# Kernel tuning notes

Measured on AMD Instinct MI355X. Metric: run time of the kernel, lower is better.

The kernel has to match this reference:

```python
import jax, jax.numpy as jnp
import numpy as np

B, N, D, E, ET, L = 2, 50000, 64, 400000, 200000, 6
R_STRUCT = 4
EPS = 1e-5


def _ln(x, g, b):
    m = jnp.mean(x, axis=-1, keepdims=True)
    v = jnp.mean((x - m) ** 2, axis=-1, keepdims=True)
    return (x - m) * jax.lax.rsqrt(v + EPS) * g + b


def _nbf(boundary, src, dst, rel_e_fn, W, b, g, beta):
    # One RelNBFNet / TextRelNBFNet stack of GeneralizedRelationalConv layers:
    #   distmult message, sum aggregation with boundary self-loop message,
    #   linear([x, agg]) -> layernorm -> relu, short_cut residual.
    # boundary: [B, N, D]
    x = boundary
    for i in range(W.shape[0]):
        msg = x[:, src, :] * rel_e_fn(i)                    # [B, E, D]
        agg = jnp.zeros_like(x).at[:, dst, :].add(msg) + boundary
        h = jnp.concatenate([x, agg], axis=-1) @ W[i] + b[i]
        h = jax.nn.relu(_ln(h, g[i], beta[i]))
        x = h + x                                           # short_cut
    return x


def setup_inputs() -> dict:
    key = jax.random.key(0)
    ks = jax.random.split(key, 16)
    s = 0.05
    return {
        "rel_text_init": jax.random.normal(ks[0], (N, D), jnp.float32),
        "struct_rel": jax.random.normal(ks[1], (L, R_STRUCT, D), jnp.float32) * s,
        "struct_W": jax.random.normal(ks[2], (L, 2 * D, D), jnp.float32) * s,
        "struct_b": jnp.zeros((L, D), jnp.float32),
        "struct_g": jnp.ones((L, D), jnp.float32),
        "struct_beta": jnp.zeros((L, D), jnp.float32),
        "text_rel": jax.random.normal(ks[3], (L, 1, D), jnp.float32) * s,
        "text_W": jax.random.normal(ks[4], (L, 2 * D, D), jnp.float32) * s,
        "text_b": jnp.zeros((L, D), jnp.float32),
        "text_g": jnp.ones((L, D), jnp.float32),
        "text_beta": jnp.zeros((L, D), jnp.float32),
        "fuse_W1": jax.random.normal(ks[5], (2 * D, D), jnp.float32) * s,
        "fuse_b1": jnp.zeros((D,), jnp.float32),
        "fuse_W2": jax.random.normal(ks[6], (D, D), jnp.float32) * s,
        "fuse_b2": jnp.zeros((D,), jnp.float32),
        "h_index": jax.random.randint(ks[7], (B,), 0, N),
        "edge_index": jax.random.randint(ks[8], (2, E), 0, N),
        "edge_type": jax.random.randint(ks[9], (E,), 0, R_STRUCT),
        "text_edge_index": jax.random.randint(ks[10], (2, ET), 0, N),
    }


def reference(rel_text_init, struct_rel, struct_W, struct_b, struct_g, struct_beta,
              text_rel, text_W, text_b, text_g, text_beta,
              fuse_W1, fuse_b1, fuse_W2, fuse_b2,
              h_index, edge_index, edge_type, text_edge_index):
    # struct branch: boundary = indicator at query relation node
    boundary_s = jnp.zeros((B, N, D), rel_text_init.dtype).at[jnp.arange(B), h_index].add(1.0)
    h = _nbf(boundary_s, edge_index[0], edge_index[1],
             lambda i: struct_rel[i][edge_type],
             struct_W, struct_b, struct_g, struct_beta)
    # text branch: boundary = text-derived init features, single relation type
    boundary_t = jnp.broadcast_to(rel_text_init[None], (B, N, D))
    z = _nbf(boundary_t, text_edge_index[0], text_edge_index[1],
             lambda i: text_rel[i, 0][None, None, :],
             text_W, text_b, text_g, text_beta)
    # mlp fusion (alpha = 1.0)
    f = jax.nn.relu(jnp.concatenate([h, z], axis=-1) @ fuse_W1 + fuse_b1)
    return f @ fuse_W2 + fuse_b2
```

## Files before the change

kernel.cpp:

```cpp
#include <hip/hip_runtime.h>


#define FMA4R(v, wbase, R0, R1, R2, R3) do {                                  \
    const float4* _w = (const float4*)(wbase); float4 _t;                     \
    _t=_w[0]; R0.x=fmaf(v,_t.x,R0.x); R0.y=fmaf(v,_t.y,R0.y); R0.z=fmaf(v,_t.z,R0.z); R0.w=fmaf(v,_t.w,R0.w); \
    _t=_w[1]; R1.x=fmaf(v,_t.x,R1.x); R1.y=fmaf(v,_t.y,R1.y); R1.z=fmaf(v,_t.z,R1.z); R1.w=fmaf(v,_t.w,R1.w); \
    _t=_w[2]; R2.x=fmaf(v,_t.x,R2.x); R2.y=fmaf(v,_t.y,R2.y); R2.z=fmaf(v,_t.z,R2.z); R2.w=fmaf(v,_t.w,R2.w); \
    _t=_w[3]; R3.x=fmaf(v,_t.x,R3.x); R3.y=fmaf(v,_t.y,R3.y); R3.z=fmaf(v,_t.z,R3.z); R3.w=fmaf(v,_t.w,R3.w); \
} while (0)

#define SUM4(Ai) ((Ai.x + Ai.y) + (Ai.z + Ai.w))
#define VAR4(Ai) do { float _c;                                               \
    _c = Ai.x - m; vs = fmaf(_c, _c, vs); _c = Ai.y - m; vs = fmaf(_c, _c, vs); \
    _c = Ai.z - m; vs = fmaf(_c, _c, vs); _c = Ai.w - m; vs = fmaf(_c, _c, vs); \
} while (0)

#define RSEL(ty) (((ty) < 2) ? ((ty) == 0 ? r0 : r1) : ((ty) == 2 ? r2 : r3))

__global__ __launch_bounds__(256) void k_init_onehot(
    float* __restrict__ x, const int* __restrict__ h_index, int N, int total)
{
    int idx = blockIdx.x * 256 + threadIdx.x;
    if (idx >= total) return;
    int row = idx >> 6;
    int b = row / N;
    int n = row - b * N;
    x[idx] = (n == h_index[b]) ? 1.0f : 0.0f;
}

__global__ __launch_bounds__(256) void k_hist(
    const int* __restrict__ dst, int* __restrict__ cnt, int E)
{
    int e = blockIdx.x * 256 + threadIdx.x;
    if (e < E) atomicAdd(&cnt[dst[e]], 1);
}

__global__ __launch_bounds__(1024) void k_scan_blk(
    const int* __restrict__ cnt, int* __restrict__ off,
    int* __restrict__ bsum, int n)
{
    __shared__ int wsum[16], wpre[16], tot;
    int tid = threadIdx.x, lane = tid & 63, w = tid >> 6;
    int i = blockIdx.x * 1024 + tid;
    int v = (i < n) ? cnt[i] : 0;
    int s = v;
    #pragma unroll
    for (int d = 1; d < 64; d <<= 1) {
        int t = __shfl_up(s, d);
        if (lane >= d) s += t;
    }
    if (lane == 63) wsum[w] = s;
    __syncthreads();
    if (w == 0 && lane < 16) {
        int ws = wsum[lane];
        int p = ws;
        #pragma unroll
        for (int d = 1; d < 16; d <<= 1) {
            int t = __shfl_up(p, d);
            if (lane >= d) p += t;
        }
        wpre[lane] = p - ws;
        if (lane == 15) tot = p;
    }
    __syncthreads();
    if (i < n) off[i + 1] = wpre[w] + s;
    if (tid == 0) {
        bsum[blockIdx.x] = tot;
        if (blockIdx.x == 0) off[0] = 0;
    }
}

__global__ __launch_bounds__(1024) void k_scan_top(int* __restrict__ bsum, int nb)
{
    __shared__ int wsum[16], wpre[16];
    int tid = threadIdx.x, lane = tid & 63, w = tid >> 6;
    int v = (tid < nb) ? bsum[tid] : 0;
    int s = v;
    #pragma unroll
    for (int d = 1; d < 64; d <<= 1) {
        int t = __shfl_up(s, d);
        if (lane >= d) s += t;
    }
    if (lane == 63) wsum[w] = s;
    __syncthreads();
    if (w == 0 && lane < 16) {
        int ws = wsum[lane];
        int p = ws;
        #pragma unroll
        for (int d = 1; d < 16; d <<= 1) {
            int t = __shfl_up(p, d);
            if (lane >= d) p += t;
        }
        wpre[lane] = p - ws;
    }
    __syncthreads();
    if (tid < nb) bsum[tid] = wpre[w] + s - v;
}

__global__ __launch_bounds__(1024) void k_scan_add(
    const int* __restrict__ bsum, int* __restrict__ off, int n)
{
    int i = blockIdx.x * 1024 + threadIdx.x;
    if (i < n) off[i + 1] += bsum[blockIdx.x];
}

__global__ __launch_bounds__(256) void k_fill(
    const int* __restrict__ src, const int* __restrict__ dst,
    const int* __restrict__ etype,
    const int* __restrict__ off, int* __restrict__ cnt,
    int* __restrict__ packed, int E)
{
    int e = blockIdx.x * 256 + threadIdx.x;
    if (e >= E) return;
    int d = dst[e];
    int pos = off[d] + atomicSub(&cnt[d], 1) - 1;
    int ty = etype ? etype[e] : 0;
    packed[pos] = src[e] | (ty << 27);
}

__global__ __launch_bounds__(256) void k_gather_struct2(
    const float* __restrict__ x, float* __restrict__ agg,
    const int* __restrict__ off, const int* __restrict__ packed,
    const float* __restrict__ rel,
    const int* __restrict__ h_index,
    int N)
{
    int n = (blockIdx.x * 256 + threadIdx.x) >> 6;
    int lane = threadIdx.x & 63;
    if (n >= N) return;
    float r0 = rel[lane], r1 = rel[64 + lane];
    float r2 = rel[128 + lane], r3 = rel[192 + lane];
    const float* x0 = x;
    const float* x1 = x + (size_t)N * 64;
    float acc0 = (n == h_index[0]) ? 1.0f : 0.0f;
    float acc1 = (n == h_index[1]) ? 1.0f : 0.0f;
    int p0 = __builtin_amdgcn_readfirstlane(off[n]);
    int p1 = __builtin_amdgcn_readfirstlane(off[n + 1]);
    for (int p = p0; p < p1; p += 64) {
        int myPk = (p + lane < p1) ? packed[p + lane] : 0;
        int cnt = min(p1 - p, 64);
        int i = 0;
        for (; i + 4 <= cnt; i += 4) {
            int pka = __shfl(myPk, i + 0), pkb = __shfl(myPk, i + 1);
            int pkc = __shfl(myPk, i + 2), pkd = __shfl(myPk, i + 3);
            int sa = pka & 0x03FFFFFF, ta = pka >> 27;
            int sb = pkb & 0x03FFFFFF, tb = pkb >> 27;
            int sc = pkc & 0x03FFFFFF, tc = pkc >> 27;
            int sd = pkd & 0x03FFFFFF, td = pkd >> 27;
            float ra = RSEL(ta), rb = RSEL(tb), rc = RSEL(tc), rd = RSEL(td);
            float a0 = x0[(size_t)sa * 64 + lane], a1 = x1[(size_t)sa * 64 + lane];
            float b0 = x0[(size_t)sb * 64 + lane], b1 = x1[(size_t)sb * 64 + lane];
            float c0 = x0[(size_t)sc * 64 + lane], c1 = x1[(size_t)sc * 64 + lane];
            float d0 = x0[(size_t)sd * 64 + lane], d1 = x1[(size_t)sd * 64 + lane];
            acc0 = fmaf(a0, ra, acc0); acc1 = fmaf(a1, ra, acc1);
            acc0 = fmaf(b0, rb, acc0); acc1 = fmaf(b1, rb, acc1);
            acc0 = fmaf(c0, rc, acc0); acc1 = fmaf(c1, rc, acc1);
            acc0 = fmaf(d0, rd, acc0); acc1 = fmaf(d1, rd, acc1);
        }
        for (; i < cnt; ++i) {
            int pk = __shfl(myPk, i);
            int s = pk & 0x03FFFFFF, ty = pk >> 27;
            float r = RSEL(ty);
            acc0 = fmaf(x0[(size_t)s * 64 + lane], r, acc0);
            acc1 = fmaf(x1[(size_t)s * 64 + lane], r, acc1);
        }
    }
    agg[(size_t)n * 64 + lane] = acc0;
    agg[(size_t)(N + n) * 64 + lane] = acc1;
}

__global__ __launch_bounds__(256) void k_gather_struct_gen(
    const float* __restrict__ x, float* __restrict__ agg,
    const int* __restrict__ off, const int* __restrict__ packed,
    const float* __restrict__ rel, const int* __restrict__ h_index,
    int N, int BN)
{
    int wid = (blockIdx.x * 256 + threadIdx.x) >> 6;
    int lane = threadIdx.x & 63;
    if (wid >= BN) return;
    int b = wid / N;
    int n = wid - b * N;
    float r0 = rel[lane], r1 = rel[64 + lane];
    float r2 = rel[128 + lane], r3 = rel[192 + lane];
    const float* xb = x + (size_t)b * N * 64;
    float acc = (n == h_index[b]) ? 1.0f : 0.0f;
    int p0 = off[n], p1 = off[n + 1];
    for (int p = p0; p < p1; ++p) {
        int pk = packed[p];
        int s = pk & 0x03FFFFFF, ty = pk >> 27;
        acc = fmaf(xb[(size_t)s * 64 + lane], RSEL(ty), acc);
    }
    agg[(size_t)wid * 64 + lane] = acc;
}

__global__ __launch_bounds__(256) void k_gather_text(
    const float* __restrict__ x, float* __restrict__ agg,
    const int* __restrict__ off, const int* __restrict__ packed,
    const float* __restrict__ rel,
    const float* __restrict__ init,
    int N)
{
    int n = (blockIdx.x * 256 + threadIdx.x) >> 6;
    int lane = threadIdx.x & 63;
    if (n >= N) return;
    float r = rel[lane];
    float acc = init[(size_t)n * 64 + lane];
    float acc2 = 0.f;
    int p0 = __builtin_amdgcn_readfirstlane(off[n]);
    int p1 = __builtin_amdgcn_readfirstlane(off[n + 1]);
    for (int p = p0; p < p1; p += 64) {
        int myPk = (p + lane < p1) ? packed[p + lane] : 0;
        int cnt = min(p1 - p, 64);
        int i = 0;
        for (; i + 4 <= cnt; i += 4) {
            int sa = __shfl(myPk, i + 0), sb = __shfl(myPk, i + 1);
            int sc = __shfl(myPk, i + 2), sd = __shfl(myPk, i + 3);
            float a = x[(size_t)sa * 64 + lane];
            float b = x[(size_t)sb * 64 + lane];
            float c = x[(size_t)sc * 64 + lane];
            float d = x[(size_t)sd * 64 + lane];
            acc = fmaf(a, r, acc);  acc2 = fmaf(b, r, acc2);
            acc = fmaf(c, r, acc);  acc2 = fmaf(d, r, acc2);
        }
        for (; i < cnt; ++i) {
            int s = __shfl(myPk, i);
            acc = fmaf(x[(size_t)s * 64 + lane], r, acc);
        }
    }
    agg[(size_t)n * 64 + lane] = acc + acc2;
}

__global__ __launch_bounds__(256) void k_update(
    const float* __restrict__ W,
    const float* __restrict__ bias, const float* __restrict__ g,
    const float* __restrict__ beta,
    float* __restrict__ x, const float* __restrict__ agg, int rows)
{
    __shared__ float Wl[128 * 64];
    __shared__ float bl[64], gl[64], bel[64];
    int tid = threadIdx.x;
    {
        const float4* W4 = (const float4*)W;
        float4* Wl4 = (float4*)Wl;
        #pragma unroll
        for (int i = 0; i < 8; ++i) Wl4[tid + i * 256] = W4[tid + i * 256];
        if (tid < 64) { bl[tid] = bias[tid]; gl[tid] = g[tid]; bel[tid] = beta[tid]; }
    }
    __syncthreads();

    int gt = blockIdx.x * 256 + tid;
    int row = gt >> 2;
    int jc = (gt & 3) * 16;
    if (row >= rows) return;
    const float* xr = x + (size_t)row * 64;
    const float* ar = agg + (size_t)row * 64;

    const float4* bj = (const float4*)(bl + jc);
    float4 A0 = bj[0], A1 = bj[1], A2 = bj[2], A3 = bj[3];

    #pragma unroll
    for (int kb = 0; kb < 64; kb += 4) {
        float4 iv = *(const float4*)(xr + kb);
        FMA4R(iv.x, Wl + (kb + 0) * 64 + jc, A0, A1, A2, A3);
        FMA4R(iv.y, Wl + (kb + 1) * 64 + jc, A0, A1, A2, A3);
        FMA4R(iv.z, Wl + (kb + 2) * 64 + jc, A0, A1, A2, A3);
        FMA4R(iv.w, Wl + (kb + 3) * 64 + jc, A0, A1, A2, A3);
    }
    #pragma unroll
    for (int kb = 0; kb < 64; kb += 4) {
        float4 iv = *(const float4*)(ar + kb);
        FMA4R(iv.x, Wl + (64 + kb + 0) * 64 + jc, A0, A1, A2, A3);
        FMA4R(iv.y, Wl + (64 + kb + 1) * 64 + jc, A0, A1, A2, A3);
        FMA4R(iv.z, Wl + (64 + kb + 2) * 64 + jc, A0, A1, A2, A3);
        FMA4R(iv.w, Wl + (64 + kb + 3) * 64 + jc, A0, A1, A2, A3);
    }

    float ls = SUM4(A0) + SUM4(A1) + SUM4(A2) + SUM4(A3);
    ls += __shfl_xor(ls, 1);
    ls += __shfl_xor(ls, 2);
    float m = ls * (1.0f / 64.0f);
    float vs = 0.f;
    VAR4(A0); VAR4(A1); VAR4(A2); VAR4(A3);
    vs += __shfl_xor(vs, 1);
    vs += __shfl_xor(vs, 2);
    float inv = rsqrtf(vs * (1.0f / 64.0f) + 1e-5f);

    float* xw = x + (size_t)row * 64 + jc;
    const float4* gg4 = (const float4*)(gl + jc);
    const float4* bb4 = (const float4*)(bel + jc);
    const float4* xv4 = (const float4*)(xr + jc);
    #define OUTC(Aj, c) do {                                                  \
        float4 xv = xv4[c]; float4 gg = gg4[c]; float4 bb = bb4[c];           \
        float4 y;                                                             \
        y.x = fmaxf((Aj.x - m) * inv * gg.x + bb.x, 0.f) + xv.x;              \
        y.y = fmaxf((Aj.y - m) * inv * gg.y + bb.y, 0.f) + xv.y;              \
        y.z = fmaxf((Aj.z - m) * inv * gg.z + bb.z, 0.f) + xv.z;              \
        y.w = fmaxf((Aj.w - m) * inv * gg.w + bb.w, 0.f) + xv.w;              \
        ((float4*)xw)[c] = y; } while (0)
    OUTC(A0, 0); OUTC(A1, 1); OUTC(A2, 2); OUTC(A3, 3);
    #undef OUTC
}

__global__ __launch_bounds__(256) void k_fuse(
    const float* __restrict__ W1, const float* __restrict__ b1,
    const float* __restrict__ W2, const float* __restrict__ b2,
    float* __restrict__ out, const float* __restrict__ z, int N, int rows)
{
    __shared__ float W1l[128 * 64];
    __shared__ float W2l[64 * 64];
    __shared__ float b1l[64], b2l[64];
    int tid = threadIdx.x;
    {
        const float4* Wa = (const float4*)W1;
        float4* Wla = (float4*)W1l;
        #pragma unroll
        for (int i = 0; i < 8; ++i) Wla[tid + i * 256] = Wa[tid + i * 256];
        const float4* Wb = (const float4*)W2;
        float4* Wlb = (float4*)W2l;
        #pragma unroll
        for (int i = 0; i < 4; ++i) Wlb[tid + i * 256] = Wb[tid + i * 256];
        if (tid < 64) { b1l[tid] = b1[tid]; b2l[tid] = b2[tid]; }
    }
    __syncthreads();

    int gt = blockIdx.x * 256 + tid;
    int row = gt >> 2;
    int q = gt & 3;
    int jc = q * 16;
    if (row >= rows) return;
    int n = row % N;
    const float* hr = out + (size_t)row * 64;
    const float* zr = z + (size_t)n * 64;
    int lane = tid & 63;

    const float4* bj = (const float4*)(b1l + jc);
    float4 F0 = bj[0], F1 = bj[1], F2 = bj[2], F3 = bj[3];
    #pragma unroll
    for (int kb = 0; kb < 64; kb += 4) {
        float4 iv = *(const float4*)(hr + kb);
        FMA4R(iv.x, W1l + (kb + 0) * 64 + jc, F0, F1, F2, F3);
        FMA4R(iv.y, W1l + (kb + 1) * 64 + jc, F0, F1, F2, F3);
        FMA4R(iv.z, W1l + (kb + 2) * 64 + jc, F0, F1, F2, F3);
        FMA4R(iv.w, W1l + (kb + 3) * 64 + jc, F0, F1, F2, F3);
    }
    #pragma unroll
    for (int kb = 0; kb < 64; kb += 4) {
        float4 iv = *(const float4*)(zr + kb);
        FMA4R(iv.x, W1l + (64 + kb + 0) * 64 + jc, F0, F1, F2, F3);
        FMA4R(iv.y, W1l + (64 + kb + 1) * 64 + jc, F0, F1, F2, F3);
        FMA4R(iv.z, W1l + (64 + kb + 2) * 64 + jc, F0, F1, F2, F3);
        FMA4R(iv.w, W1l + (64 + kb + 3) * 64 + jc, F0, F1, F2, F3);
    }
    F0.x = fmaxf(F0.x, 0.f); F0.y = fmaxf(F0.y, 0.f); F0.z = fmaxf(F0.z, 0.f); F0.w = fmaxf(F0.w, 0.f);
    F1.x = fmaxf(F1.x, 0.f); F1.y = fmaxf(F1.y, 0.f); F1.z = fmaxf(F1.z, 0.f); F1.w = fmaxf(F1.w, 0.f);
    F2.x = fmaxf(F2.x, 0.f); F2.y = fmaxf(F2.y, 0.f); F2.z = fmaxf(F2.z, 0.f); F2.w = fmaxf(F2.w, 0.f);
    F3.x = fmaxf(F3.x, 0.f); F3.y = fmaxf(F3.y, 0.f); F3.z = fmaxf(F3.z, 0.f); F3.w = fmaxf(F3.w, 0.f);

    const float4* bj2 = (const float4*)(b2l + jc);
    float4 O0 = bj2[0], O1 = bj2[1], O2 = bj2[2], O3 = bj2[3];
    int srcLane = (lane & ~3) | ((q + 1) & 3);
    #pragma unroll
    for (int s = 0; s < 4; ++s) {
        int c = (q + s) & 3;
        const float* w2 = W2l + (c * 16) * 64 + jc;
        FMA4R(F0.x, w2 + 0 * 64,  O0, O1, O2, O3);
        FMA4R(F0.y, w2 + 1 * 64,  O0, O1, O2, O3);
        FMA4R(F0.z, w2 + 2 * 64,  O0, O1, O2, O3);
        FMA4R(F0.w, w2 + 3 * 64,  O0, O1, O2, O3);
        FMA4R(F1.x, w2 + 4 * 64,  O0, O1, O2, O3);
        FMA4R(F1.y, w2 + 5 * 64,  O0, O1, O2, O3);
        FMA4R(F1.z, w2 + 6 * 64,  O0, O1, O2, O3);
        FMA4R(F1.w, w2 + 7 * 64,  O0, O1, O2, O3);
        FMA4R(F2.x, w2 + 8 * 64,  O0, O1, O2, O3);
        FMA4R(F2.y, w2 + 9 * 64,  O0, O1, O2, O3);
        FMA4R(F2.z, w2 + 10 * 64, O0, O1, O2, O3);
        FMA4R(F2.w, w2 + 11 * 64, O0, O1, O2, O3);
        FMA4R(F3.x, w2 + 12 * 64, O0, O1, O2, O3);
        FMA4R(F3.y, w2 + 13 * 64, O0, O1, O2, O3);
        FMA4R(F3.z, w2 + 14 * 64, O0, O1, O2, O3);
        FMA4R(F3.w, w2 + 15 * 64, O0, O1, O2, O3);
        if (s < 3) {
            F0.x = __shfl(F0.x, srcLane); F0.y = __shfl(F0.y, srcLane);
            F0.z = __shfl(F0.z, srcLane); F0.w = __shfl(F0.w, srcLane);
            F1.x = __shfl(F1.x, srcLane); F1.y = __shfl(F1.y, srcLane);
            F1.z = __shfl(F1.z, srcLane); F1.w = __shfl(F1.w, srcLane);
            F2.x = __shfl(F2.x, srcLane); F2.y = __shfl(F2.y, srcLane);
            F2.z = __shfl(F2.z, srcLane); F2.w = __shfl(F2.w, srcLane);
            F3.x = __shfl(F3.x, srcLane); F3.y = __shfl(F3.y, srcLane);
            F3.z = __shfl(F3.z, srcLane); F3.w = __shfl(F3.w, srcLane);
        }
    }
    float4* ow4 = (float4*)(out + (size_t)row * 64 + jc);
    ow4[0] = O0; ow4[1] = O1; ow4[2] = O2; ow4[3] = O3;
}

extern "C" void kernel_launch(void* const* d_in, const int* in_sizes, int n_in,
                              void* d_out, int out_size, void* d_ws, size_t ws_size,
                              hipStream_t stream)
{
    const float* rel_text_init = (const float*)d_in[0];
    const float* struct_rel    = (const float*)d_in[1];
    const float* struct_W      = (const float*)d_in[2];
    const float* struct_b      = (const float*)d_in[3];
    const float* struct_g      = (const float*)d_in[4];
    const float* struct_beta   = (const float*)d_in[5];
    const float* text_rel      = (const float*)d_in[6];
    const float* text_W        = (const float*)d_in[7];
    const float* text_b        = (const float*)d_in[8];
    const float* text_g        = (const float*)d_in[9];
    const float* text_beta     = (const float*)d_in[10];
    const float* fuse_W1       = (const float*)d_in[11];
    const float* fuse_b1       = (const float*)d_in[12];
    const float* fuse_W2       = (const float*)d_in[13];
    const float* fuse_b2       = (const float*)d_in[14];
    const int*   h_index       = (const int*)d_in[15];
    const int*   edge_index    = (const int*)d_in[16];
    const int*   edge_type     = (const int*)d_in[17];
    const int*   text_edge_idx = (const int*)d_in[18];

    const int B  = in_sizes[15];
    const int N  = in_sizes[0] / 64;
    const int E  = in_sizes[17];
    const int ET = in_sizes[18] / 2;
    const int L  = in_sizes[3] / 64;
    const int R  = in_sizes[1] / (L * 64);

    const int* src  = edge_index;
    const int* dst  = edge_index + E;
    const int* tsrc = text_edge_idx;
    const int* tdst = text_edge_idx + ET;

    float* x_t   = (float*)d_ws;
    float* agg_t = x_t + (size_t)N * 64;
    float* agg_s = agg_t + (size_t)N * 64;
    int*   cnt_s = (int*)(agg_s + (size_t)B * N * 64);
    int*   off_s = cnt_s + N;
    int*   pk_s  = off_s + N + 1;
    int*   cnt_t = pk_s + E;
    int*   off_t = cnt_t + N;
    int*   pk_t  = off_t + N + 1;
    int*   bsum_s = pk_t + ET;
    int*   bsum_t = bsum_s + 1024;

    float* x_s = (float*)d_out;

    const size_t nd  = (size_t)N * 64;
    const int rows_s = B * N;
    const int tot_s  = rows_s * 64;
    const int nb     = (N + 1023) / 1024;

    const int gb_init   = (tot_s + 255) / 256;
    const int gb_e      = (E + 255) / 256;
    const int gb_et     = (ET + 255) / 256;
    const int gb_wave_n = (N * 64 + 255) / 256;
    const int gb_upd_s  = (rows_s * 4 + 255) / 256;
    const int gb_upd_t  = (N * 4 + 255) / 256;
    const int gb_fuse   = (rows_s * 4 + 255) / 256;

    hipMemsetAsync(cnt_s, 0, (size_t)N * 4, stream);
    hipMemsetAsync(cnt_t, 0, (size_t)N * 4, stream);
    k_hist<<<gb_e, 256, 0, stream>>>(dst, cnt_s, E);
    k_hist<<<gb_et, 256, 0, stream>>>(tdst, cnt_t, ET);
    k_scan_blk<<<nb, 1024, 0, stream>>>(cnt_s, off_s, bsum_s, N);
    k_scan_blk<<<nb, 1024, 0, stream>>>(cnt_t, off_t, bsum_t, N);
    k_scan_top<<<1, 1024, 0, stream>>>(bsum_s, nb);
    k_scan_top<<<1, 1024, 0, stream>>>(bsum_t, nb);
    k_scan_add<<<nb, 1024, 0, stream>>>(bsum_s, off_s, N);
    k_scan_add<<<nb, 1024, 0, stream>>>(bsum_t, off_t, N);
    k_fill<<<gb_e, 256, 0, stream>>>(src, dst, edge_type, off_s, cnt_s, pk_s, E);
    k_fill<<<gb_et, 256, 0, stream>>>(tsrc, tdst, nullptr, off_t, cnt_t, pk_t, ET);

    k_init_onehot<<<gb_init, 256, 0, stream>>>(x_s, h_index, N, tot_s);
    for (int i = 0; i < L; ++i) {
        if (B == 2) {
            k_gather_struct2<<<gb_wave_n, 256, 0, stream>>>(
                x_s, agg_s, off_s, pk_s,
                struct_rel + (size_t)i * R * 64, h_index, N);
        } else {
            k_gather_struct_gen<<<(rows_s * 64 + 255) / 256, 256, 0, stream>>>(
                x_s, agg_s, off_s, pk_s,
                struct_rel + (size_t)i * R * 64, h_index, N, rows_s);
        }
        k_update<<<gb_upd_s, 256, 0, stream>>>(
            struct_W + (size_t)i * 128 * 64, struct_b + i * 64,
            struct_g + i * 64, struct_beta + i * 64, x_s, agg_s, rows_s);
    }

    hipMemcpyAsync(x_t, rel_text_init, nd * sizeof(float),
                   hipMemcpyDeviceToDevice, stream);
    for (int i = 0; i < L; ++i) {
        k_gather_text<<<gb_wave_n, 256, 0, stream>>>(
            x_t, agg_t, off_t, pk_t,
            text_rel + (size_t)i * 64, rel_text_init, N);
        k_update<<<gb_upd_t, 256, 0, stream>>>(
            text_W + (size_t)i * 128 * 64, text_b + i * 64,
            text_g + i * 64, text_beta + i * 64, x_t, agg_t, N);
    }

    k_fuse<<<gb_fuse, 256, 0, stream>>>(
        fuse_W1, fuse_b1, fuse_W2, fuse_b2, x_s, x_t, N, rows_s);
}
```

Before: 800.2 us.

## Co-launch struct and text branches per layer and process two rows per thread

Measured after the change: 956.8 us. +19.6%, slower.

```diff
diff --git a/kernel.cpp b/kernel.cpp
--- a/kernel.cpp
+++ b/kernel.cpp
@@ -9,10 +9,26 @@
     _t=_w[3]; R3.x=fmaf(v,_t.x,R3.x); R3.y=fmaf(v,_t.y,R3.y); R3.z=fmaf(v,_t.z,R3.z); R3.w=fmaf(v,_t.w,R3.w); \
 } while (0)
 
+#define FMA4R2(v0, v1, wbase, P0,P1,P2,P3, Q0,Q1,Q2,Q3) do {                  \
+    const float4* _w = (const float4*)(wbase); float4 _t;                     \
+    _t=_w[0];                                                                 \
+    P0.x=fmaf(v0,_t.x,P0.x); P0.y=fmaf(v0,_t.y,P0.y); P0.z=fmaf(v0,_t.z,P0.z); P0.w=fmaf(v0,_t.w,P0.w); \
+    Q0.x=fmaf(v1,_t.x,Q0.x); Q0.y=fmaf(v1,_t.y,Q0.y); Q0.z=fmaf(v1,_t.z,Q0.z); Q0.w=fmaf(v1,_t.w,Q0.w); \
+    _t=_w[1];                                                                 \
+    P1.x=fmaf(v0,_t.x,P1.x); P1.y=fmaf(v0,_t.y,P1.y); P1.z=fmaf(v0,_t.z,P1.z); P1.w=fmaf(v0,_t.w,P1.w); \
+    Q1.x=fmaf(v1,_t.x,Q1.x); Q1.y=fmaf(v1,_t.y,Q1.y); Q1.z=fmaf(v1,_t.z,Q1.z); Q1.w=fmaf(v1,_t.w,Q1.w); \
+    _t=_w[2];                                                                 \
+    P2.x=fmaf(v0,_t.x,P2.x); P2.y=fmaf(v0,_t.y,P2.y); P2.z=fmaf(v0,_t.z,P2.z); P2.w=fmaf(v0,_t.w,P2.w); \
+    Q2.x=fmaf(v1,_t.x,Q2.x); Q2.y=fmaf(v1,_t.y,Q2.y); Q2.z=fmaf(v1,_t.z,Q2.z); Q2.w=fmaf(v1,_t.w,Q2.w); \
+    _t=_w[3];                                                                 \
+    P3.x=fmaf(v0,_t.x,P3.x); P3.y=fmaf(v0,_t.y,P3.y); P3.z=fmaf(v0,_t.z,P3.z); P3.w=fmaf(v0,_t.w,P3.w); \
+    Q3.x=fmaf(v1,_t.x,Q3.x); Q3.y=fmaf(v1,_t.y,Q3.y); Q3.z=fmaf(v1,_t.z,Q3.z); Q3.w=fmaf(v1,_t.w,Q3.w); \
+} while (0)
+
 #define SUM4(Ai) ((Ai.x + Ai.y) + (Ai.z + Ai.w))
-#define VAR4(Ai) do { float _c;                                               \
-    _c = Ai.x - m; vs = fmaf(_c, _c, vs); _c = Ai.y - m; vs = fmaf(_c, _c, vs); \
-    _c = Ai.z - m; vs = fmaf(_c, _c, vs); _c = Ai.w - m; vs = fmaf(_c, _c, vs); \
+#define VAR4M(Ai, mm, vv) do { float _c;                                      \
+    _c = Ai.x - mm; vv = fmaf(_c, _c, vv); _c = Ai.y - mm; vv = fmaf(_c, _c, vv); \
+    _c = Ai.z - mm; vv = fmaf(_c, _c, vv); _c = Ai.w - mm; vv = fmaf(_c, _c, vv); \
 } while (0)
 
 #define RSEL(ty) (((ty) < 2) ? ((ty) == 0 ? r0 : r1) : ((ty) == 2 ? r2 : r3))
@@ -28,20 +44,29 @@
     x[idx] = (n == h_index[b]) ? 1.0f : 0.0f;
 }
 
-__global__ __launch_bounds__(256) void k_hist(
-    const int* __restrict__ dst, int* __restrict__ cnt, int E)
-{
-    int e = blockIdx.x * 256 + threadIdx.x;
-    if (e < E) atomicAdd(&cnt[dst[e]], 1);
-}
-
-__global__ __launch_bounds__(1024) void k_scan_blk(
-    const int* __restrict__ cnt, int* __restrict__ off,
-    int* __restrict__ bsum, int n)
-{
+__global__ __launch_bounds__(256) void k_hist_all(
+    const int* __restrict__ dst_s, const int* __restrict__ dst_t,
+    int* __restrict__ cnt_s, int* __restrict__ cnt_t, int E, int ET)
+{
+    int i = blockIdx.x * 256 + threadIdx.x;
+    if (i < E) atomicAdd(&cnt_s[dst_s[i]], 1);
+    else if (i < E + ET) atomicAdd(&cnt_t[dst_t[i - E]], 1);
+}
+
+__global__ __launch_bounds__(1024) void k_scan_blk2(
+    const int* __restrict__ cnt_s, int* __restrict__ off_s, int* __restrict__ bsum_s,
+    const int* __restrict__ cnt_t, int* __restrict__ off_t, int* __restrict__ bsum_t,
+    int n, int nb)
+{
+    bool tpath = blockIdx.x >= nb;
+    int lb = tpath ? blockIdx.x - nb : blockIdx.x;
+    const int* cnt = tpath ? cnt_t : cnt_s;
+    int* off = tpath ? off_t : off_s;
+    int* bsum = tpath ? bsum_t : bsum_s;
+
     __shared__ int wsum[16], wpre[16], tot;
     int tid = threadIdx.x, lane = tid & 63, w = tid >> 6;
-    int i = blockIdx.x * 1024 + tid;
+    int i = lb * 1024 + tid;
     int v = (i < n) ? cnt[i] : 0;
     int s = v;
     #pragma unroll
@@ -65,13 +90,15 @@
     __syncthreads();
     if (i < n) off[i + 1] = wpre[w] + s;
     if (tid == 0) {
-        bsum[blockIdx.x] = tot;
-        if (blockIdx.x == 0) off[0] = 0;
-    }
-}
-
-__global__ __launch_bounds__(1024) void k_scan_top(int* __restrict__ bsum, int nb)
-{
+        bsum[lb] = tot;
+        if (lb == 0) off[0] = 0;
+    }
+}
+
+__global__ __launch_bounds__(1024) void k_scan_top2(
+    int* __restrict__ bsum_s, int* __restrict__ bsum_t, int nb)
+{
+    int* bsum = (blockIdx.x == 0) ? bsum_s : bsum_t;
     __shared__ int wsum[16], wpre[16];
     int tid = threadIdx.x, lane = tid & 63, w = tid >> 6;
     int v = (tid < nb) ? bsum[tid] : 0;
@@ -97,76 +124,128 @@
     if (tid < nb) bsum[tid] = wpre[w] + s - v;
 }
 
-__global__ __launch_bounds__(1024) void k_scan_add(
-    const int* __restrict__ bsum, int* __restrict__ off, int n)
-{
-    int i = blockIdx.x * 1024 + threadIdx.x;
-    if (i < n) off[i + 1] += bsum[blockIdx.x];
-}
-
-__global__ __launch_bounds__(256) void k_fill(
-    const int* __restrict__ src, const int* __restrict__ dst,
+__global__ __launch_bounds__(1024) void k_scan_add2(
+    const int* __restrict__ bsum_s, int* __restrict__ off_s,
+    const int* __restrict__ bsum_t, int* __restrict__ off_t, int n, int nb)
+{
+    bool tpath = blockIdx.x >= nb;
+    int lb = tpath ? blockIdx.x - nb : blockIdx.x;
+    int i = lb * 1024 + threadIdx.x;
+    if (i < n) (tpath ? off_t : off_s)[i + 1] += (tpath ? bsum_t : bsum_s)[lb];
+}
+
+__global__ __launch_bounds__(256) void k_fill_all(
+    const int* __restrict__ src_s, const int* __restrict__ dst_s,
     const int* __restrict__ etype,
-    const int* __restrict__ off, int* __restrict__ cnt,
-    int* __restrict__ packed, int E)
-{
-    int e = blockIdx.x * 256 + threadIdx.x;
-    if (e >= E) return;
-    int d = dst[e];
-    int pos = off[d] + atomicSub(&cnt[d], 1) - 1;
-    int ty = etype ? etype[e] : 0;
-    packed[pos] = src[e] | (ty << 27);
-}
-
-__global__ __launch_bounds__(256) void k_gather_struct2(
-    const float* __restrict__ x, float* __restrict__ agg,
-    const int* __restrict__ off, const int* __restrict__ packed,
-    const float* __restrict__ rel,
-    const int* __restrict__ h_index,
-    int N)
-{
-    int n = (blockIdx.x * 256 + threadIdx.x) >> 6;
-    int lane = threadIdx.x & 63;
+    const int* __restrict__ off_s, int* __restrict__ cnt_s, int* __restrict__ pk_s,
+    const int* __restrict__ src_t, const int* __restrict__ dst_t,
+    const int* __restrict__ off_t, int* __restrict__ cnt_t, int* __restrict__ pk_t,
+    int E, int ET)
+{
+    int i = blockIdx.x * 256 + threadIdx.x;
+    if (i < E) {
+        int d = dst_s[i];
+        int pos = off_s[d] + atomicSub(&cnt_s[d], 1) - 1;
+        pk_s[pos] = src_s[i] | (etype[i] << 27);
+    } else if (i < E + ET) {
+        int e = i - E;
+        int d = dst_t[e];
+        int pos = off_t[d] + atomicSub(&cnt_t[d], 1) - 1;
+        pk_t[pos] = src_t[e];
+    }
+}
+
+__global__ __launch_bounds__(256) void k_gather_all(
+    const float* __restrict__ xs, float* __restrict__ aggs,
+    const int* __restrict__ offs, const int* __restrict__ pks,
+    const float* __restrict__ rels,
+    const int* __restrict__ hidx,
+    const float* __restrict__ xt, float* __restrict__ aggt,
+    const int* __restrict__ offt, const int* __restrict__ pkt,
+    const float* __restrict__ relt,
+    const float* __restrict__ init,
+    int N, int sblocks, int tblocks)
+{
+    int tid = threadIdx.x;
+    int lane = tid & 63;
+    bool isStruct; int lb;
+    if (sblocks == tblocks) { isStruct = !(blockIdx.x & 1); lb = blockIdx.x >> 1; }
+    else if ((int)blockIdx.x < sblocks) { isStruct = true; lb = blockIdx.x; }
+    else { isStruct = false; lb = blockIdx.x - sblocks; }
+    int n = (lb * 256 + tid) >> 6;
     if (n >= N) return;
-    float r0 = rel[lane], r1 = rel[64 + lane];
-    float r2 = rel[128 + lane], r3 = rel[192 + lane];
-    const float* x0 = x;
-    const float* x1 = x + (size_t)N * 64;
-    float acc0 = (n == h_index[0]) ? 1.0f : 0.0f;
-    float acc1 = (n == h_index[1]) ? 1.0f : 0.0f;
-    int p0 = __builtin_amdgcn_readfirstlane(off[n]);
-    int p1 = __builtin_amdgcn_readfirstlane(off[n + 1]);
-    for (int p = p0; p < p1; p += 64) {
-        int myPk = (p + lane < p1) ? packed[p + lane] : 0;
-        int cnt = min(p1 - p, 64);
-        int i = 0;
-        for (; i + 4 <= cnt; i += 4) {
-            int pka = __shfl(myPk, i + 0), pkb = __shfl(myPk, i + 1);
-            int pkc = __shfl(myPk, i + 2), pkd = __shfl(myPk, i + 3);
-            int sa = pka & 0x03FFFFFF, ta = pka >> 27;
-            int sb = pkb & 0x03FFFFFF, tb = pkb >> 27;
-            int sc = pkc & 0x03FFFFFF, tc = pkc >> 27;
-            int sd = pkd & 0x03FFFFFF, td = pkd >> 27;
-            float ra = RSEL(ta), rb = RSEL(tb), rc = RSEL(tc), rd = RSEL(td);
-            float a0 = x0[(size_t)sa * 64 + lane], a1 = x1[(size_t)sa * 64 + lane];
-            float b0 = x0[(size_t)sb * 64 + lane], b1 = x1[(size_t)sb * 64 + lane];
-            float c0 = x0[(size_t)sc * 64 + lane], c1 = x1[(size_t)sc * 64 + lane];
-            float d0 = x0[(size_t)sd * 64 + lane], d1 = x1[(size_t)sd * 64 + lane];
-            acc0 = fmaf(a0, ra, acc0); acc1 = fmaf(a1, ra, acc1);
-            acc0 = fmaf(b0, rb, acc0); acc1 = fmaf(b1, rb, acc1);
-            acc0 = fmaf(c0, rc, acc0); acc1 = fmaf(c1, rc, acc1);
-            acc0 = fmaf(d0, rd, acc0); acc1 = fmaf(d1, rd, acc1);
+
+    if (isStruct) {
+        float r0 = rels[lane], r1 = rels[64 + lane];
+        float r2 = rels[128 + lane], r3 = rels[192 + lane];
+        const float* x0 = xs;
+        const float* x1 = xs + (size_t)N * 64;
+        float acc0 = (n == hidx[0]) ? 1.0f : 0.0f;
+        float acc1 = (n == hidx[1]) ? 1.0f : 0.0f;
+        int p0 = __builtin_amdgcn_readfirstlane(offs[n]);
+        int p1 = __builtin_amdgcn_readfirstlane(offs[n + 1]);
+        for (int p = p0; p < p1; p += 64) {
+            int myPk = (p + lane < p1) ? pks[p + lane] : 0;
+            int cnt = min(p1 - p, 64);
+            int i = 0;
+            for (; i + 4 <= cnt; i += 4) {
+                int pka = __shfl(myPk, i + 0), pkb = __shfl(myPk, i + 1);
+                int pkc = __shfl(myPk, i + 2), pkd = __shfl(myPk, i + 3);
+                int sa = pka & 0x03FFFFFF, ta = pka >> 27;
+                int sb = pkb & 0x03FFFFFF, tb = pkb >> 27;
+                int sc = pkc & 0x03FFFFFF, tc = pkc >> 27;
+                int sd = pkd & 0x03FFFFFF, td = pkd >> 27;
+                float ra = RSEL(ta), rb = RSEL(tb), rc = RSEL(tc), rd = RSEL(td);
+                float a0 = x0[(size_t)sa * 64 + lane], a1 = x1[(size_t)sa * 64 + lane];
+                float b0 = x0[(size_t)sb * 64 + lane], b1 = x1[(size_t)sb * 64 + lane];
+                float c0 = x0[(size_t)sc * 64 + lane], c1 = x1[(size_t)sc * 64 + lane];
+                float d0 = x0[(size_t)sd * 64 + lane], d1 = x1[(size_t)sd * 64 + lane];
+                acc0 = fmaf(a0, ra, acc0); acc1 = fmaf(a1, ra, acc1);
+                acc0 = fmaf(b0, rb, acc0); acc1 = fmaf(b1, rb, acc1);
+                acc0 = fmaf(c0, rc, acc0); acc1 = fmaf(c1, rc, acc1);
+                acc0 = fmaf(d0, rd, acc0); acc1 = fmaf(d1, rd, acc1);
+            }
+            for (; i < cnt; ++i) {
+                int pk = __shfl(myPk, i);
+                int s = pk & 0x03FFFFFF, ty = pk >> 27;
+                float r = RSEL(ty);
+                acc0 = fmaf(x0[(size_t)s * 64 + lane], r, acc0);
+                acc1 = fmaf(x1[(size_t)s * 64 + lane], r, acc1);
+            }
         }
-        for (; i < cnt; ++i) {
-            int pk = __shfl(myPk, i);
-            int s = pk & 0x03FFFFFF, ty = pk >> 27;
-            float r = RSEL(ty);
-            acc0 = fmaf(x0[(size_t)s * 64 + lane], r, acc0);
-            acc1 = fmaf(x1[(size_t)s * 64 + lane], r, acc1);
+        aggs[(size_t)n * 64 + lane] = acc0;
+        aggs[(size_t)(N + n) * 64 + lane] = acc1;
+    } else {
+        float r = relt[lane];
+        float acc = init[(size_t)n * 64 + lane];
+        float acc2 = 0.f;
+        int p0 = __builtin_amdgcn_readfirstlane(offt[n]);
+        int p1 = __builtin_amdgcn_readfirstlane(offt[n + 1]);
+        for (int p = p0; p < p1; p += 64) {
+            int myPk = (p + lane < p1) ? pkt[p + lane] : 0;
+            int cnt = min(p1 - p, 64);
+            int i = 0;
+            for (; i + 8 <= cnt; i += 8) {
+                int s0 = __shfl(myPk, i + 0), s1 = __shfl(myPk, i + 1);
+                int s2 = __shfl(myPk, i + 2), s3 = __shfl(myPk, i + 3);
+                int s4 = __shfl(myPk, i + 4), s5 = __shfl(myPk, i + 5);
+                int s6 = __shfl(myPk, i + 6), s7 = __shfl(myPk, i + 7);
+                float a = xt[(size_t)s0 * 64 + lane], b = xt[(size_t)s1 * 64 + lane];
+                float c = xt[(size_t)s2 * 64 + lane], d = xt[(size_t)s3 * 64 + lane];
+                float e = xt[(size_t)s4 * 64 + lane], f = xt[(size_t)s5 * 64 + lane];
+                float g = xt[(size_t)s6 * 64 + lane], h = xt[(size_t)s7 * 64 + lane];
+                acc = fmaf(a, r, acc);  acc2 = fmaf(b, r, acc2);
+                acc = fmaf(c, r, acc);  acc2 = fmaf(d, r, acc2);
+                acc = fmaf(e, r, acc);  acc2 = fmaf(f, r, acc2);
+                acc = fmaf(g, r, acc);  acc2 = fmaf(h, r, acc2);
+            }
+            for (; i < cnt; ++i) {
+                int s = __shfl(myPk, i);
+                acc = fmaf(xt[(size_t)s * 64 + lane], r, acc);
+            }
         }
-    }
-    agg[(size_t)n * 64 + lane] = acc0;
-    agg[(size_t)(N + n) * 64 + lane] = acc1;
+        aggt[(size_t)n * 64 + lane] = acc + acc2;
+    }
 }
 
 __global__ __launch_bounds__(256) void k_gather_struct_gen(
@@ -193,49 +272,31 @@
     agg[(size_t)wid * 64 + lane] = acc;
 }
 
-__global__ __launch_bounds__(256) void k_gather_text(
-    const float* __restrict__ x, float* __restrict__ agg,
-    const int* __restrict__ off, const int* __restrict__ packed,
-    const float* __restrict__ rel,
-    const float* __restrict__ init,
-    int N)
-{
-    int n = (blockIdx.x * 256 + threadIdx.x) >> 6;
-    int lane = threadIdx.x & 63;
-    if (n >= N) return;
-    float r = rel[lane];
-    float acc = init[(size_t)n * 64 + lane];
-    float acc2 = 0.f;
-    int p0 = __builtin_amdgcn_readfirstlane(off[n]);
-    int p1 = __builtin_amdgcn_readfirstlane(off[n + 1]);
-    for (int p = p0; p < p1; p += 64) {
-        int myPk = (p + lane < p1) ? packed[p + lane] : 0;
-        int cnt = min(p1 - p, 64);
-        int i = 0;
-        for (; i + 4 <= cnt; i += 4) {
-            int sa = __shfl(myPk, i + 0), sb = __shfl(myPk, i + 1);
-            int sc = __shfl(myPk, i + 2), sd = __shfl(myPk, i + 3);
-            float a = x[(size_t)sa * 64 + lane];
-            float b = x[(size_t)sb * 64 + lane];
-            float c = x[(size_t)sc * 64 + lane];
-            float d = x[(size_t)sd * 64 + lane];
-            acc = fmaf(a, r, acc);  acc2 = fmaf(b, r, acc2);
-            acc = fmaf(c, r, acc);  acc2 = fmaf(d, r, acc2);
-        }
-        for (; i < cnt; ++i) {
-            int s = __shfl(myPk, i);
-            acc = fmaf(x[(size_t)s * 64 + lane], r, acc);
-        }
-    }
-    agg[(size_t)n * 64 + lane] = acc + acc2;
-}
-
-__global__ __launch_bounds__(256) void k_update(
-    const float* __restrict__ W,
-    const float* __restrict__ bias, const float* __restrict__ g,
-    const float* __restrict__ beta,
-    float* __restrict__ x, const float* __restrict__ agg, int rows)
-{
+__global__ __launch_bounds__(256) void k_update_all(
+    const float* __restrict__ Ws, const float* __restrict__ bs_,
+    const float* __restrict__ gs, const float* __restrict__ betas,
+    float* __restrict__ xs, const float* __restrict__ aggs, int rows_s,
+    const float* __restrict__ Wt, const float* __restrict__ bt_,
+    const float* __restrict__ gt_, const float* __restrict__ betat,
+    float* __restrict__ xt, const float* __restrict__ aggt, int rows_t,
+    int bs_blocks, int bt_blocks)
+{
+    bool tpath; int lb;
+    if (bs_blocks == 2 * bt_blocks) {
+        int m3 = blockIdx.x % 3, d3 = blockIdx.x / 3;
+        if (m3 != 2) { tpath = false; lb = d3 * 2 + m3; }
+        else { tpath = true; lb = d3; }
+    } else if ((int)blockIdx.x < bs_blocks) { tpath = false; lb = blockIdx.x; }
+    else { tpath = true; lb = blockIdx.x - bs_blocks; }
+
+    const float* W    = tpath ? Wt : Ws;
+    const float* bias = tpath ? bt_ : bs_;
+    const float* g    = tpath ? gt_ : gs;
+    const float* beta = tpath ? betat : betas;
+    float* x          = tpath ? xt : xs;
+    const float* agg  = tpath ? aggt : aggs;
+    int rows          = tpath ? rows_t : rows_s;
+
     __shared__ float Wl[128 * 64];
     __shared__ float bl[64], gl[64], bel[64];
     int tid = threadIdx.x;
@@ -248,56 +309,72 @@
     }
     __syncthreads();
 
-    int gt = blockIdx.x * 256 + tid;
-    int row = gt >> 2;
-    int jc = (gt & 3) * 16;
-    if (row >= rows) return;
-    const float* xr = x + (size_t)row * 64;
-    const float* ar = agg + (size_t)row * 64;
+    int gt2 = lb * 256 + tid;
+    int pair = gt2 >> 2;
+    int q = gt2 & 3, jc = q * 16;
+    int r0i = pair * 2, r1i = r0i + 1;
+    if (r0i >= rows) return;
+    bool h1 = (r1i < rows);
+    const float* xr0 = x + (size_t)r0i * 64;
+    const float* ar0 = agg + (size_t)r0i * 64;
+    const float* xr1 = h1 ? x + (size_t)r1i * 64 : xr0;
+    const float* ar1 = h1 ? agg + (size_t)r1i * 64 : ar0;
 
     const float4* bj = (const float4*)(bl + jc);
     float4 A0 = bj[0], A1 = bj[1], A2 = bj[2], A3 = bj[3];
+    float4 B0 = bj[0], B1 = bj[1], B2 = bj[2], B3 = bj[3];
 
     #pragma unroll
     for (int kb = 0; kb < 64; kb += 4) {
-        float4 iv = *(const float4*)(xr + kb);
-        FMA4R(iv.x, Wl + (kb + 0) * 64 + jc, A0, A1, A2, A3);
-        FMA4R(iv.y, Wl + (kb + 1) * 64 + jc, A0, A1, A2, A3);
-        FMA4R(iv.z, Wl + (kb + 2) * 64 + jc, A0, A1, A2, A3);
-        FMA4R(iv.w, Wl + (kb + 3) * 64 + jc, A0, A1, A2, A3);
+        float4 i0 = *(const float4*)(xr0 + kb);
+        float4 i1 = *(const float4*)(xr1 + kb);
+        FMA4R2(i0.x, i1.x, Wl + (kb + 0) * 64 + jc, A0,A1,A2,A3, B0,B1,B2,B3);
+        FMA4R2(i0.y, i1.y, Wl + (kb + 1) * 64 + jc, A0,A1,A2,A3, B0,B1,B2,B3);
+        FMA4R2(i0.z, i1.z, Wl + (kb + 2) * 64 + jc, A0,A1,A2,A3, B0,B1,B2,B3);
+        FMA4R2(i0.w, i1.w, Wl + (kb + 3) * 64 + jc, A0,A1,A2,A3, B0,B1,B2,B3);
     }
     #pragma unroll
     for (int kb = 0; kb < 64; kb += 4) {
-        float4 iv = *(const float4*)(ar + kb);
-        FMA4R(iv.x, Wl + (64 + kb + 0) * 64 + jc, A0, A1, A2, A3);
-        FMA4R(iv.y, Wl + (64 + kb + 1) * 64 + jc, A0, A1, A2, A3);
-        FMA4R(iv.z, Wl + (64 + kb + 2) * 64 + jc, A0, A1, A2, A3);
-        FMA4R(iv.w, Wl + (64 + kb + 3) * 64 + jc, A0, A1, A2, A3);
-    }
-
-    float ls = SUM4(A0) + SUM4(A1) + SUM4(A2) + SUM4(A3);
-    ls += __shfl_xor(ls, 1);
-    ls += __shfl_xor(ls, 2);
-    float m = ls * (1.0f / 64.0f);
-    float vs = 0.f;
-    VAR4(A0); VAR4(A1); VAR4(A2); VAR4(A3);
-    vs += __shfl_xor(vs, 1);
-    vs += __shfl_xor(vs, 2);
-    float inv = rsqrtf(vs * (1.0f / 64.0f) + 1e-5f);
-
-    float* xw = x + (size_t)row * 64 + jc;
+        float4 i0 = *(const float4*)(ar0 + kb);
+        float4 i1 = *(const float4*)(ar1 + kb);
+        FMA4R2(i0.x, i1.x, Wl + (64 + kb + 0) * 64 + jc, A0,A1,A2,A3, B0,B1,B2,B3);
+        FMA4R2(i0.y, i1.y, Wl + (64 + kb + 1) * 64 + jc, A0,A1,A2,A3, B0,B1,B2,B3);
+        FMA4R2(i0.z, i1.z, Wl + (64 + kb + 2) * 64 + jc, A0,A1,A2,A3, B0,B1,B2,B3);
+        FMA4R2(i0.w, i1.w, Wl + (64 + kb + 3) * 64 + jc, A0,A1,A2,A3, B0,B1,B2,B3);
+    }
+
+    float ls0 = SUM4(A0) + SUM4(A1) + SUM4(A2) + SUM4(A3);
+    float ls1 = SUM4(B0) + SUM4(B1) + SUM4(B2) + SUM4(B3);
+    ls0 += __shfl_xor(ls0, 1); ls0 += __shfl_xor(ls0, 2);
+    ls1 += __shfl_xor(ls1, 1); ls1 += __shfl_xor(ls1, 2);
+    float m0 = ls0 * (1.0f / 64.0f), m1 = ls1 * (1.0f / 64.0f);
+    float v0 = 0.f, v1 = 0.f;
+    VAR4M(A0, m0, v0); VAR4M(A1, m0, v0); VAR4M(A2, m0, v0); VAR4M(A3, m0, v0);
+    VAR4M(B0, m1, v1); VAR4M(B1, m1, v1); VAR4M(B2, m1, v1); VAR4M(B3, m1, v1);
+    v0 += __shfl_xor(v0, 1); v0 += __shfl_xor(v0, 2);
+    v1 += __shfl_xor(v1, 1); v1 += __shfl_xor(v1, 2);
+    float inv0 = rsqrtf(v0 * (1.0f / 64.0f) + 1e-5f);
+    float inv1 = rsqrtf(v1 * (1.0f / 64.0f) + 1e-5f);
+
     const float4* gg4 = (const float4*)(gl + jc);
     const float4* bb4 = (const float4*)(bel + jc);
-    const float4* xv4 = (const float4*)(xr + jc);
-    #define OUTC(Aj, c) do {                                                  \
-        float4 xv = xv4[c]; float4 gg = gg4[c]; float4 bb = bb4[c];           \
+    #define OUTC(Aj, c, mm, iv, xrp, xwp) do {                                \
+        float4 xv = ((const float4*)(xrp))[c];                                \
+        float4 gg = gg4[c]; float4 bb = bb4[c];                               \
         float4 y;                                                             \
-        y.x = fmaxf((Aj.x - m) * inv * gg.x + bb.x, 0.f) + xv.x;              \
-        y.y = fmaxf((Aj.y - m) * inv * gg.y + bb.y, 0.f) + xv.y;              \
-        y.z = fmaxf((Aj.z - m) * inv * gg.z + bb.z, 0.f) + xv.z;              \
-        y.w = fmaxf((Aj.w - m) * inv * gg.w + bb.w, 0.f) + xv.w;              \
-        ((float4*)xw)[c] = y; } while (0)
-    OUTC(A0, 0); OUTC(A1, 1); OUTC(A2, 2); OUTC(A3, 3);
+        y.x = fmaxf((Aj.x - mm) * iv * gg.x + bb.x, 0.f) + xv.x;              \
+        y.y = fmaxf((Aj.y - mm) * iv * gg.y + bb.y, 0.f) + xv.y;              \
+        y.z = fmaxf((Aj.z - mm) * iv * gg.z + bb.z, 0.f) + xv.z;              \
+        y.w = fmaxf((Aj.w - mm) * iv * gg.w + bb.w, 0.f) + xv.w;              \
+        ((float4*)(xwp))[c] = y; } while (0)
+    float* xw0 = x + (size_t)r0i * 64 + jc;
+    OUTC(A0, 0, m0, inv0, xr0 + jc, xw0); OUTC(A1, 1, m0, inv0, xr0 + jc, xw0);
+    OUTC(A2, 2, m0, inv0, xr0 + jc, xw0); OUTC(A3, 3, m0, inv0, xr0 + jc, xw0);
+    if (h1) {
+        float* xw1 = x + (size_t)r1i * 64 + jc;
+        OUTC(B0, 0, m1, inv1, xr1 + jc, xw1); OUTC(B1, 1, m1, inv1, xr1 + jc, xw1);
+        OUTC(B2, 2, m1, inv1, xr1 + jc, xw1); OUTC(B3, 3, m1, inv1, xr1 + jc, xw1);
+    }
     #undef OUTC
 }
 
@@ -323,75 +400,95 @@
     }
     __syncthreads();
 
-    int gt = blockIdx.x * 256 + tid;
-    int row = gt >> 2;
-    int q = gt & 3;
-    int jc = q * 16;
-    if (row >= rows) return;
-    int n = row % N;
-    const float* hr = out + (size_t)row * 64;
-    const float* zr = z + (size_t)n * 64;
+    int gt2 = blockIdx.x * 256 + tid;
+    int pair = gt2 >> 2;
+    int q = gt2 & 3, jc = q * 16;
+    int r0i = pair * 2, r1i = r0i + 1;
+    if (r0i >= rows) return;
+    bool h1 = (r1i < rows);
     int lane = tid & 63;
+    int n0 = r0i % N, n1 = r1i % N;
+    const float* hr0 = out + (size_t)r0i * 64;
+    const float* zr0 = z + (size_t)n0 * 64;
+    const float* hr1 = h1 ? out + (size_t)r1i * 64 : hr0;
+    const float* zr1 = h1 ? z + (size_t)n1 * 64 : zr0;
 
     const float4* bj = (const float4*)(b1l + jc);
-    float4 F0 = bj[0], F1 = bj[1], F2 = bj[2], F3 = bj[3];
+    float4 FA0 = bj[0], FA1 = bj[1], FA2 = bj[2], FA3 = bj[3];
+    float4 FB0 = bj[0], FB1 = bj[1], FB2 = bj[2], FB3 = bj[3];
     #pragma unroll
     for (int kb = 0; kb < 64; kb += 4) {
-        float4 iv = *(const float4*)(hr + kb);
-        FMA4R(iv.x, W1l + (kb + 0) * 64 + jc, F0, F1, F2, F3);
-        FMA4R(iv.y, W1l + (kb + 1) * 64 + jc, F0, F1, F2, F3);
-        FMA4R(iv.z, W1l + (kb + 2) * 64 + jc, F0, F1, F2, F3);
-        FMA4R(iv.w, W1l + (kb + 3) * 64 + jc, F0, F1, F2, F3);
+        float4 i0 = *(const float4*)(hr0 + kb);
+        float4 i1 = *(const float4*)(hr1 + kb);
+        FMA4R2(i0.x, i1.x, W1l + (kb + 0) * 64 + jc, FA0,FA1,FA2,FA3, FB0,FB1,FB2,FB3);
+        FMA4R2(i0.y, i1.y, W1l + (kb + 1) * 64 + jc, FA0,FA1,FA2,FA3, FB0,FB1,FB2,FB3);
+        FMA4R2(i0.z, i1.z, W1l + (kb + 2) * 64 + jc, FA0,FA1,FA2,FA3, FB0,FB1,FB2,FB3);
+        FMA4R2(i0.w, i1.w, W1l + (kb + 3) * 64 + jc, FA0,FA1,FA2,FA3, FB0,FB1,FB2,FB3);
     }
     #pragma unroll
     for (int kb = 0; kb < 64; kb += 4) {
-        float4 iv = *(const float4*)(zr + kb);
-        FMA4R(iv.x, W1l + (64 + kb + 0) * 64 + jc, F0, F1, F2, F3);
-        FMA4R(iv.y, W1l + (64 + kb + 1) * 64 + jc, F0, F1, F2, F3);
-        FMA4R(iv.z, W1l + (64 + kb + 2) * 64 + jc, F0, F1, F2, F3);
-        FMA4R(iv.w, W1l + (64 + kb + 3) * 64 + jc, F0, F1, F2, F3);
-    }
-    F0.x = fmaxf(F0.x, 0.f); F0.y = fmaxf(F0.y, 0.f); F0.z = fmaxf(F0.z, 0.f); F0.w = fmaxf(F0.w, 0.f);
-    F1.x = fmaxf(F1.x, 0.f); F1.y = fmaxf(F1.y, 0.f); F1.z = fmaxf(F1.z, 0.f); F1.w = fmaxf(F1.w, 0.f);
-    F2.x = fmaxf(F2.x, 0.f); F2.y = fmaxf(F2.y, 0.f); F2.z = fmaxf(F2.z, 0.f); F2.w = fmaxf(F2.w, 0.f);
-    F3.x = fmaxf(F3.x, 0.f); F3.y = fmaxf(F3.y, 0.f); F3.z = fmaxf(F3.z, 0.f); F3.w = fmaxf(F3.w, 0.f);
+        float4 i0 = *(const float4*)(zr0 + kb);
+        float4 i1 = *(const float4*)(zr1 + kb);
+        FMA4R2(i0.x, i1.x, W1l + (64 + kb + 0) * 64 + jc, FA0,FA1,FA2,FA3, FB0,FB1,FB2,FB3);
+        FMA4R2(i0.y, i1.y, W1l + (64 + kb + 1) * 64 + jc, FA0,FA1,FA2,FA3, FB0,FB1,FB2,FB3);
+        FMA4R2(i0.z, i1.z, W1l + (64 + kb + 2) * 64 + jc, FA0,FA1,FA2,FA3, FB0,FB1,FB2,FB3);
+        FMA4R2(i0.w, i1.w, W1l + (64 + kb + 3) * 64 + jc, FA0,FA1,FA2,FA3, FB0,FB1,FB2,FB3);
+    }
+    #define RELU4(Ai) do { Ai.x = fmaxf(Ai.x, 0.f); Ai.y = fmaxf(Ai.y, 0.f); \
+                           Ai.z = fmaxf(Ai.z, 0.f); Ai.w = fmaxf(Ai.w, 0.f); } while (0)
+    RELU4(FA0); RELU4(FA1); RELU4(FA2); RELU4(FA3);
+    RELU4(FB0); RELU4(FB1); RELU4(FB2); RELU4(FB3);
+    #undef RELU4
 
     const float4* bj2 = (const float4*)(b2l + jc);
-    float4 O0 = bj2[0], O1 = bj2[1], O2 = bj2[2], O3 = bj2[3];
+    float4 OA0 = bj2[0], OA1 = bj2[1], OA2 = bj2[2], OA3 = bj2[3];
+    float4 OB0 = bj2[0], OB1 = bj2[1], OB2 = bj2[2], OB3 = bj2[3];
     int srcLane = (lane & ~3) | ((q + 1) & 3);
     #pragma unroll
     for (int s = 0; s < 4; ++s) {
         int c = (q + s) & 3;
         const float* w2 = W2l + (c * 16) * 64 + jc;
-        FMA4R(F0.x, w2 + 0 * 64,  O0, O1, O2, O3);
-        FMA4R(F0.y, w2 + 1 * 64,  O0, O1, O2, O3);
-        FMA4R(F0.z, w2 + 2 * 64,  O0, O1, O2, O3);
-        FMA4R(F0.w, w2 + 3 * 64,  O0, O1, O2, O3);
-        FMA4R(F1.x, w2 + 4 * 64,  O0, O1, O2, O3);
-        FMA4R(F1.y, w2 + 5 * 64,  O0, O1, O2, O3);
-        FMA4R(F1.z, w2 + 6 * 64,  O0, O1, O2, O3);
-        FMA4R(F1.w, w2 + 7 * 64,  O0, O1, O2, O3);
-        FMA4R(F2.x, w2 + 8 * 64,  O0, O1, O2, O3);
-        FMA4R(F2.y, w2 + 9 * 64,  O0, O1, O2, O3);
-        FMA4R(F2.z, w2 + 10 * 64, O0, O1, O2, O3);
-        FMA4R(F2.w, w2 + 11 * 64, O0, O1, O2, O3);
-        FMA4R(F3.x, w2 + 12 * 64, O0, O1, O2, O3);
-        FMA4R(F3.y, w2 + 13 * 64, O0, O1, O2, O3);
-        FMA4R(F3.z, w2 + 14 * 64, O0, O1, O2, O3);
-        FMA4R(F3.w, w2 + 15 * 64, O0, O1, O2, O3);
+        FMA4R2(FA0.x, FB0.x, w2 + 0 * 64,  OA0,OA1,OA2,OA3, OB0,OB1,OB2,OB3);
+        FMA4R2(FA0.y, FB0.y, w2 + 1 * 64,  OA0,OA1,OA2,OA3, OB0,OB1,OB2,OB3);
+        FMA4R2(FA0.z, FB0.z, w2 + 2 * 64,  OA0,OA1,OA2,OA3, OB0,OB1,OB2,OB3);
+        FMA4R2(FA0.w, FB0.w, w2 + 3 * 64,  OA0,OA1,OA2,OA3, OB0,OB1,OB2,OB3);
+        FMA4R2(FA1.x, FB1.x, w2 + 4 * 64,  OA0,OA1,OA2,OA3, OB0,OB1,OB2,OB3);
+        FMA4R2(FA1.y, FB1.y, w2 + 5 * 64,  OA0,OA1,OA2,OA3, OB0,OB1,OB2,OB3);
+        FMA4R2(FA1.z, FB1.z, w2 + 6 * 64,  OA0,OA1,OA2,OA3, OB0,OB1,OB2,OB3);
+        FMA4R2(FA1.w, FB1.w, w2 + 7 * 64,  OA0,OA1,OA2,OA3, OB0,OB1,OB2,OB3);
+        FMA4R2(FA2.x, FB2.x, w2 + 8 * 64,  OA0,OA1,OA2,OA3, OB0,OB1,OB2,OB3);
+        FMA4R2(FA2.y, FB2.y, w2 + 9 * 64,  OA0,OA1,OA2,OA3, OB0,OB1,OB2,OB3);
+        FMA4R2(FA2.z, FB2.z, w2 + 10 * 64, OA0,OA1,OA2,OA3, OB0,OB1,OB2,OB3);
+        FMA4R2(FA2.w, FB2.w, w2 + 11 * 64, OA0,OA1,OA2,OA3, OB0,OB1,OB2,OB3);
+        FMA4R2(FA3.x, FB3.x, w2 + 12 * 64, OA0,OA1,OA2,OA3, OB0,OB1,OB2,OB3);
+        FMA4R2(FA3.y, FB3.y, w2 + 13 * 64, OA0,OA1,OA2,OA3, OB0,OB1,OB2,OB3);
+        FMA4R2(FA3.z, FB3.z, w2 + 14 * 64, OA0,OA1,OA2,OA3, OB0,OB1,OB2,OB3);
+        FMA4R2(FA3.w, FB3.w, w2 + 15 * 64, OA0,OA1,OA2,OA3, OB0,OB1,OB2,OB3);
         if (s < 3) {
-            F0.x = __shfl(F0.x, srcLane); F0.y = __shfl(F0.y, srcLane);
-            F0.z = __shfl(F0.z, srcLane); F0.w = __shfl(F0.w, srcLane);
-            F1.x = __shfl(F1.x, srcLane); F1.y = __shfl(F1.y, srcLane);
-            F1.z = __shfl(F1.z, srcLane); F1.w = __shfl(F1.w, srcLane);
-            F2.x = __shfl(F2.x, srcLane); F2.y = __shfl(F2.y, srcLane);
-            F2.z = __shfl(F2.z, srcLane); F2.w = __shfl(F2.w, srcLane);
-            F3.x = __shfl(F3.x, srcLane); F3.y = __shfl(F3.y, srcLane);
-            F3.z = __shfl(F3.z, srcLane); F3.w = __shfl(F3.w, srcLane);
+            FA0.x = __shfl(FA0.x, srcLane); FA0.y = __shfl(FA0.y, srcLane);
+            FA0.z = __shfl(FA0.z, srcLane); FA0.w = __shfl(FA0.w, srcLane);
+            FA1.x = __shfl(FA1.x, srcLane); FA1.y = __shfl(FA1.y, srcLane);
+            FA1.z = __shfl(FA1.z, srcLane); FA1.w = __shfl(FA1.w, srcLane);
+            FA2.x = __shfl(FA2.x, srcLane); FA2.y = __shfl(FA2.y, srcLane);
+            FA2.z = __shfl(FA2.z, srcLane); FA2.w = __shfl(FA2.w, srcLane);
+            FA3.x = __shfl(FA3.x, srcLane); FA3.y = __shfl(FA3.y, srcLane);
+            FA3.z = __shfl(FA3.z, srcLane); FA3.w = __shfl(FA3.w, srcLane);
+            FB0.x = __shfl(FB0.x, srcLane); FB0.y = __shfl(FB0.y, srcLane);
+            FB0.z = __shfl(FB0.z, srcLane); FB0.w = __shfl(FB0.w, srcLane);
+            FB1.x = __shfl(FB1.x, srcLane); FB1.y = __shfl(FB1.y, srcLane);
+            FB1.z = __shfl(FB1.z, srcLane); FB1.w = __shfl(FB1.w, srcLane);
+            FB2.x = __shfl(FB2.x, srcLane); FB2.y = __shfl(FB2.y, srcLane);
+            FB2.z = __shfl(FB2.z, srcLane); FB2.w = __shfl(FB2.w, srcLane);
+            FB3.x = __shfl(FB3.x, srcLane); FB3.y = __shfl(FB3.y, srcLane);
+            FB3.z = __shfl(FB3.z, srcLane); FB3.w = __shfl(FB3.w, srcLane);
         }
     }
-    float4* ow4 = (float4*)(out + (size_t)row * 64 + jc);
-    ow4[0] = O0; ow4[1] = O1; ow4[2] = O2; ow4[3] = O3;
+    float4* ow0 = (float4*)(out + (size_t)r0i * 64 + jc);
+    ow0[0] = OA0; ow0[1] = OA1; ow0[2] = OA2; ow0[3] = OA3;
+    if (h1) {
+        float4* ow1 = (float4*)(out + (size_t)r1i * 64 + jc);
+        ow1[0] = OB0; ow1[1] = OB1; ow1[2] = OB2; ow1[3] = OB3;
+    }
 }
 
 extern "C" void kernel_launch(void* const* d_in, const int* in_sizes, int n_in,
@@ -450,51 +547,49 @@
     const int nb     = (N + 1023) / 1024;
 
     const int gb_init   = (tot_s + 255) / 256;
-    const int gb_e      = (E + 255) / 256;
-    const int gb_et     = (ET + 255) / 256;
+    const int gb_hist   = (E + ET + 255) / 256;
     const int gb_wave_n = (N * 64 + 255) / 256;
-    const int gb_upd_s  = (rows_s * 4 + 255) / 256;
-    const int gb_upd_t  = (N * 4 + 255) / 256;
-    const int gb_fuse   = (rows_s * 4 + 255) / 256;
+    const int pairs_s   = (rows_s + 1) / 2;
+    const int pairs_t   = (N + 1) / 2;
+    const int bs_blocks = (pairs_s * 4 + 255) / 256;
+    const int bt_blocks = (pairs_t * 4 + 255) / 256;
+    const int gb_fuse   = bs_blocks;
 
     hipMemsetAsync(cnt_s, 0, (size_t)N * 4, stream);
     hipMemsetAsync(cnt_t, 0, (size_t)N * 4, stream);
-    k_hist<<<gb_e, 256, 0, stream>>>(dst, cnt_s, E);
-    k_hist<<<gb_et, 256, 0, stream>>>(tdst, cnt_t, ET);
-    k_scan_blk<<<nb, 1024, 0, stream>>>(cnt_s, off_s, bsum_s, N);
-    k_scan_blk<<<nb, 1024, 0, stream>>>(cnt_t, off_t, bsum_t, N);
-    k_scan_top<<<1, 1024, 0, stream>>>(bsum_s, nb);
-    k_scan_top<<<1, 1024, 0, stream>>>(bsum_t, nb);
-    k_scan_add<<<nb, 1024, 0, stream>>>(bsum_s, off_s, N);
-    k_scan_add<<<nb, 1024, 0, stream>>>(bsum_t, off_t, N);
-    k_fill<<<gb_e, 256, 0, stream>>>(src, dst, edge_type, off_s, cnt_s, pk_s, E);
-    k_fill<<<gb_et, 256, 0, stream>>>(tsrc, tdst, nullptr, off_t, cnt_t, pk_t, ET);
+    k_hist_all<<<gb_hist, 256, 0, stream>>>(dst, tdst, cnt_s, cnt_t, E, ET);
+    k_scan_blk2<<<2 * nb, 1024, 0, stream>>>(cnt_s, off_s, bsum_s,
+                                             cnt_t, off_t, bsum_t, N, nb);
+    k_scan_top2<<<2, 1024, 0, stream>>>(bsum_s, bsum_t, nb);
+    k_scan_add2<<<2 * nb, 1024, 0, stream>>>(bsum_s, off_s, bsum_t, off_t, N, nb);
+    k_fill_all<<<gb_hist, 256, 0, stream>>>(src, dst, edge_type, off_s, cnt_s, pk_s,
+                                            tsrc, tdst, off_t, cnt_t, pk_t, E, ET);
 
     k_init_onehot<<<gb_init, 256, 0, stream>>>(x_s, h_index, N, tot_s);
+    hipMemcpyAsync(x_t, rel_text_init, nd * sizeof(float),
+                   hipMemcpyDeviceToDevice, stream);
+
     for (int i = 0; i < L; ++i) {
         if (B == 2) {
-            k_gather_struct2<<<gb_wave_n, 256, 0, stream>>>(
-                x_s, agg_s, off_s, pk_s,
-                struct_rel + (size_t)i * R * 64, h_index, N);
+            k_gather_all<<<2 * gb_wave_n, 256, 0, stream>>>(
+                x_s, agg_s, off_s, pk_s, struct_rel + (size_t)i * R * 64, h_index,
+                x_t, agg_t, off_t, pk_t, text_rel + (size_t)i * 64, rel_text_init,
+                N, gb_wave_n, gb_wave_n);
         } else {
             k_gather_struct_gen<<<(rows_s * 64 + 255) / 256, 256, 0, stream>>>(
                 x_s, agg_s, off_s, pk_s,
                 struct_rel + (size_t)i * R * 64, h_index, N, rows_s);
+            k_gather_all<<<gb_wave_n, 256, 0, stream>>>(
+                x_s, agg_s, off_s, pk_s, struct_rel + (size_t)i * R * 64, h_index,
+                x_t, agg_t, off_t, pk_t, text_rel + (size_t)i * 64, rel_text_init,
+                N, 0, gb_wave_n);
         }
-        k_update<<<gb_upd_s, 256, 0, stream>>>(
+        k_update_all<<<bs_blocks + bt_blocks, 256, 0, stream>>>(
             struct_W + (size_t)i * 128 * 64, struct_b + i * 64,
-            struct_g + i * 64, struct_beta + i * 64, x_s, agg_s, rows_s);
-    }
-
-    hipMemcpyAsync(x_t, rel_text_init, nd * sizeof(float),
-                   hipMemcpyDeviceToDevice, stream);
-    for (int i = 0; i < L; ++i) {
-        k_gather_text<<<gb_wave_n, 256, 0, stream>>>(
-            x_t, agg_t, off_t, pk_t,
-            text_rel + (size_t)i * 64, rel_text_init, N);
-        k_update<<<gb_upd_t, 256, 0, stream>>>(
+            struct_g + i * 64, struct_beta + i * 64, x_s, agg_s, rows_s,
             text_W + (size_t)i * 128 * 64, text_b + i * 64,
-            text_g + i * 64, text_beta + i * 64, x_t, agg_t, N);
+            text_g + i * 64, text_beta + i * 64, x_t, agg_t, N,
+            bs_blocks, bt_blocks);
     }
 
     k_fuse<<<gb_fuse, 256, 0, stream>>>(
```
